# Kernel tuning notes

Measured on AMD Instinct MI355X. Metric: run time of the kernel, lower is better.

The kernel has to match this reference:

```python
import jax, jax.numpy as jnp
import numpy as np

N = 25600          # total nodes
B = 64             # graphs in batch
NPG = N // B       # nodes per graph (400)
K = 16             # in-degree (regular graph)
E = N * K          # edges
D = 128            # hidden dim = out dim
L = 4              # DGN layers
NUM_ATOM = 128


def _linear_init(key, out_s, in_s):
    lim = 1.0 / np.sqrt(in_s)
    return jax.random.uniform(key, (out_s, in_s), jnp.float32, -lim, lim)


def setup_inputs() -> dict:
    key = jax.random.key(0)
    ks = jax.random.split(key, 16)
    node_feat = jax.random.randint(ks[0], (N,), 0, NUM_ATOM)
    # K-regular in-degree graph, edges intra-graph; dst sorted
    dst = jnp.repeat(jnp.arange(N), K)                       # [E]
    src_local = jax.random.randint(ks[1], (E,), 0, NPG)
    src = (dst // NPG) * NPG + src_local                     # same graph as dst
    eig = jax.random.normal(ks[2], (E, 2), jnp.float32)
    snorm_n = jnp.full((N, 1), 1.0 / np.sqrt(NPG), jnp.float32)
    graph_ids = jnp.arange(N) // NPG
    emb = jax.random.normal(ks[3], (NUM_ATOM, D), jnp.float32) * 0.02
    pre_W = jnp.stack([_linear_init(jax.random.fold_in(ks[4], i), D, 2 * D) for i in range(L)])
    pre_b = jnp.zeros((L, D), jnp.float32)
    post_W = jnp.stack([_linear_init(jax.random.fold_in(ks[5], i), D, 5 * D) for i in range(L)])
    post_b = jnp.zeros((L, D), jnp.float32)
    r_W0 = _linear_init(ks[6], 64, 128); r_b0 = jnp.zeros((64,), jnp.float32)
    r_W1 = _linear_init(ks[7], 32, 64);  r_b1 = jnp.zeros((32,), jnp.float32)
    r_W2 = _linear_init(ks[8], 128, 32); r_b2 = jnp.zeros((128,), jnp.float32)
    return dict(node_feat=node_feat, src=src, dst=dst, eig=eig, snorm_n=snorm_n,
                graph_ids=graph_ids, emb=emb, pre_W=pre_W, pre_b=pre_b,
                post_W=post_W, post_b=post_b, r_W0=r_W0, r_b0=r_b0,
                r_W1=r_W1, r_b1=r_b1, r_W2=r_W2, r_b2=r_b2)


def _dgn_layer(h, src, dst, eig, snorm_n, Wp, bp, Wq, bq):
    n = h.shape[0]
    # pretrans on edges: Linear(cat(h_src, h_dst))  [E, D]
    z2 = jnp.concatenate([h[src], h[dst]], axis=-1)
    e = jnp.einsum('ei,oi->eo', z2, Wp) + bp
    seg_sum = lambda v: jax.ops.segment_sum(v, dst, num_segments=n, indices_are_sorted=True)
    s = seg_sum(e)
    mean = s / K
    mx = jax.ops.segment_max(e, dst, num_segments=n, indices_are_sorted=True)
    # directional aggregator (eig_idx=1)
    w = eig[:, 1]
    denom = seg_sum(jnp.abs(w)) + 1e-8                       # [n]
    ew = w / denom[dst]                                      # [E]
    dir_agg = jnp.abs(seg_sum(e * ew[:, None]) - seg_sum(ew)[:, None] * h)
    agg = jnp.concatenate([h, mean, s, mx, dir_agg], axis=-1)  # [n, 5D]
    hn = jnp.einsum('ni,oi->no', agg, Wq) + bq
    hn = hn * snorm_n           # graph_norm
    hn = jax.nn.relu(hn)
    return h + hn               # residual (in_dim == out_dim)


def reference(node_feat, src, dst, eig, snorm_n, graph_ids, emb,
              pre_W, pre_b, post_W, post_b,
              r_W0, r_b0, r_W1, r_b1, r_W2, r_b2):
    h = emb[node_feat]                                       # AtomEncoder
    for i in range(L):
        h = _dgn_layer(h, src, dst, eig, snorm_n, pre_W[i], pre_b[i], post_W[i], post_b[i])
    # mean_nodes per graph (equal-sized graphs)
    hg = jax.ops.segment_sum(h, graph_ids, num_segments=B, indices_are_sorted=True) / NPG
    y = jax.nn.relu(hg @ r_W0.T + r_b0)
    y = jax.nn.relu(y @ r_W1.T + r_b1)
    return y @ r_W2.T + r_b2                                 # [B, 128]
```

## Files before the change

kernel.cpp:

```cpp
#include <hip/hip_runtime.h>
#include <cstddef>

#define NN 25600
#define BB 64
#define NPG 400
#define KK 16
#define LL 4

typedef _Float16 half_t;
typedef _Float16 h8 __attribute__((ext_vector_type(8)));
typedef _Float16 h4 __attribute__((ext_vector_type(4)));
typedef float f32x4 __attribute__((ext_vector_type(4)));

__global__ __launch_bounds__(256) void prep_k(const float* __restrict__ preW,
                                              const float* __restrict__ preb,
                                              const float* __restrict__ postW,
                                              half_t* __restrict__ WpreH,
                                              half_t* __restrict__ WpreL,
                                              float* __restrict__ bpre,
                                              half_t* __restrict__ WpostH,
                                              half_t* __restrict__ WpostL) {
  int idx = blockIdx.x * 256 + threadIdx.x;
  const int n1 = LL * 256 * 128;
  const int n2 = n1 + LL * 256;
  const int n3 = n2 + LL * 128 * 512;
  if (idx < n1) {
    int l = idx / 32768;
    int q = idx % 32768;
    int j = q & 7, lane = (q >> 3) & 63, kc = (q >> 9) & 3, c16 = q >> 11;
    int col = c16 * 16 + (lane & 15);
    int k = kc * 32 + (lane >> 4) * 8 + j;
    float v = (col < 128) ? preW[(size_t)l * 32768 + (size_t)col * 256 + k]
                          : preW[(size_t)l * 32768 + (size_t)(col - 128) * 256 + 128 + k];
    half_t hi = (half_t)v;
    WpreH[idx] = hi;
    WpreL[idx] = (half_t)(v - (float)hi);
  } else if (idx < n2) {
    int r = idx - n1;
    int l = r / 256, o = r % 256;
    bpre[r] = (o < 128) ? 0.f : preb[l * 128 + (o - 128)];
  } else if (idx < n3) {
    int r = idx - n2;
    int l = r / 65536;
    int q = r % 65536;
    int j = q & 7, lane = (q >> 3) & 63, kc = (q >> 9) & 15, c16 = q >> 13;
    int col = c16 * 16 + (lane & 15);
    int k = kc * 32 + (lane >> 4) * 8 + j;
    int jblk = k >> 7, kk = k & 127;
    const float* base = postW + (size_t)l * 128 * 640 + (size_t)col * 640;
    float v;
    if (jblk == 0)      v = base[kk];
    else if (jblk == 1) v = base[128 + kk] * (1.f / 16.f) + base[256 + kk];
    else if (jblk == 2) v = base[384 + kk];
    else                v = base[512 + kk];
    half_t hi = (half_t)v;
    WpostH[r] = hi;
    WpostL[r] = (half_t)(v - (float)hi);
  }
}

__global__ __launch_bounds__(256) void embed_k(const int* __restrict__ nf,
                                               const float* __restrict__ emb,
                                               float* __restrict__ hf,
                                               half_t* __restrict__ Hh,
                                               half_t* __restrict__ Hl) {
  int idx = blockIdx.x * 256 + threadIdx.x;
  int n = idx >> 5;
  int d4 = idx & 31;
  int a = nf[n];
  float4 v = *(const float4*)(emb + (size_t)a * 128 + d4 * 4);
  *(float4*)(hf + (size_t)n * 128 + d4 * 4) = v;
  h4 hi, lo;
  const float* vp = &v.x;
#pragma unroll
  for (int j = 0; j < 4; ++j) {
    half_t h = (half_t)vp[j];
    hi[j] = h;
    lo[j] = (half_t)(vp[j] - (float)h);
  }
  *(h4*)(Hh + (size_t)n * 128 + d4 * 4) = hi;
  *(h4*)(Hl + (size_t)n * 128 + d4 * 4) = lo;
}

__global__ __launch_bounds__(256) void pre_gemm_k(const half_t* __restrict__ Ah_g,
                                                  const half_t* __restrict__ Al_g,
                                                  const half_t* __restrict__ Wh_g,
                                                  const half_t* __restrict__ Wl_g,
                                                  const float* __restrict__ bias,
                                                  float* __restrict__ outF) {
  __shared__ half_t Ahs[64][132];
  __shared__ half_t Als[64][132];
  const int tid = threadIdx.x;
  const int bid = blockIdx.x;
  const int swz = (bid & 7) * 50 + (bid >> 3);
  const int r0 = swz * 64;
  const int by8 = blockIdx.y * 8;
  const int wid = tid >> 6, lane = tid & 63;
  const int wm = wid >> 1, wn = wid & 1;
  const int lr = lane & 15, lk = (lane >> 4) * 8;
  f32x4 acc[2][4] = {};

  {
    const int row = tid >> 2;
#pragma unroll
    for (int s = 0; s < 4; ++s) {
      const int koff = (tid & 3) * 8 + s * 32;
      const size_t g = (size_t)(r0 + row) * 128 + koff;
      *(h8*)&Ahs[row][koff] = *(const h8*)(Ah_g + g);
      *(h8*)&Als[row][koff] = *(const h8*)(Al_g + g);
    }
  }
  __syncthreads();

#pragma unroll
  for (int kc = 0; kc < 4; ++kc) {
    h8 af[2][2];
#pragma unroll
    for (int mi = 0; mi < 2; ++mi) {
      const int r = wm * 32 + mi * 16 + lr;
      af[mi][0] = *(const h8*)&Ahs[r][kc * 32 + lk];
      af[mi][1] = *(const h8*)&Als[r][kc * 32 + lk];
    }
#pragma unroll
    for (int nj = 0; nj < 4; ++nj) {
      const size_t fi = ((size_t)((by8 + wn * 4 + nj) * 4 + kc) * 64 + lane) * 8;
      const h8 b0v = *(const h8*)(Wh_g + fi);
      const h8 b1v = *(const h8*)(Wl_g + fi);
#pragma unroll
      for (int mi = 0; mi < 2; ++mi) {
        acc[mi][nj] = __builtin_amdgcn_mfma_f32_16x16x32_f16(af[mi][0], b0v, acc[mi][nj], 0, 0, 0);
        acc[mi][nj] = __builtin_amdgcn_mfma_f32_16x16x32_f16(af[mi][0], b1v, acc[mi][nj], 0, 0, 0);
        acc[mi][nj] = __builtin_amdgcn_mfma_f32_16x16x32_f16(af[mi][1], b0v, acc[mi][nj], 0, 0, 0);
      }
    }
  }
#pragma unroll
  for (int mi = 0; mi < 2; ++mi) {
    const int rowb = r0 + wm * 32 + mi * 16 + (lane >> 4) * 4;
#pragma unroll
    for (int nj = 0; nj < 4; ++nj) {
      const int col = by8 * 16 + wn * 64 + nj * 16 + lr;
      const float bv = bias[col];
#pragma unroll
      for (int q = 0; q < 4; ++q) {
        outF[(size_t)(rowb + q) * 256 + col] = acc[mi][nj][q] + bv;
      }
    }
  }
}

__global__ __launch_bounds__(256) void agg_post_k(const float* __restrict__ pre,
                                                  const int* __restrict__ src,
                                                  const float* __restrict__ eig,
                                                  const half_t* __restrict__ Hh,
                                                  const half_t* __restrict__ Hl,
                                                  const half_t* __restrict__ Wh,
                                                  const half_t* __restrict__ Wl,
                                                  const float* __restrict__ bias,
                                                  const float* __restrict__ snorm,
                                                  float* __restrict__ Hf,
                                                  half_t* __restrict__ Oh,
                                                  half_t* __restrict__ Ol) {
  __shared__ half_t Ah[32][392];
  __shared__ half_t Al[32][392];
  const int tid = threadIdx.x;
  const int bid = blockIdx.x;
  const int swz = (bid & 7) * 100 + (bid >> 3);
  const int r0 = swz * 32;
  const int wid = tid >> 6, lane = tid & 63;
  const int wm = wid >> 1, wn = wid & 1;
  const int lr = lane & 15, lk = (lane >> 4) * 8;

  for (int i = 0; i < 8; ++i) {
    const int lrow = wid * 8 + i;
    const int n = r0 + lrow;
    const int ebase = n * KK;
    float wv[KK];
    int sv[KK];
    float denom = 0.f;
#pragma unroll
    for (int e = 0; e < KK; ++e) {
      wv[e] = eig[(size_t)(ebase + e) * 2 + 1];
      sv[e] = src[ebase + e];
      denom += fabsf(wv[e]);
    }
    denom += 1e-8f;
    const float inv = 1.f / denom;
    float sum_ew = 0.f;
#pragma unroll
    for (int e = 0; e < KK; ++e) {
      wv[e] *= inv;
      sum_ew += wv[e];
    }
    float sA0 = 0.f, sA1 = 0.f, wA0 = 0.f, wA1 = 0.f;
    float mA0 = -3.402823466e+38f, mA1 = -3.402823466e+38f;
#pragma unroll
    for (int e = 0; e < KK; ++e) {
      const float* ap = pre + (size_t)sv[e] * 256;
      const float a0 = ap[lane];
      const float a1 = ap[64 + lane];
      sA0 += a0;
      sA1 += a1;
      wA0 = fmaf(wv[e], a0, wA0);
      wA1 = fmaf(wv[e], a1, wA1);
      mA0 = fmaxf(mA0, a0);
      mA1 = fmaxf(mA1, a1);
    }
    const float b0 = pre[(size_t)n * 256 + 128 + lane];
    const float b1 = pre[(size_t)n * 256 + 192 + lane];
    const float h0 = Hf[(size_t)n * 128 + lane];
    const float h1 = Hf[(size_t)n * 128 + 64 + lane];
    const int d0 = lane, d1 = lane + 64;
    auto wr = [&](int kcol, float v) {
      const half_t hi = (half_t)v;
      Ah[lrow][kcol] = hi;
      Al[lrow][kcol] = (half_t)(v - (float)hi);
    };
    wr(d0, sA0 + 16.f * b0);
    wr(d1, sA1 + 16.f * b1);
    wr(128 + d0, mA0 + b0);
    wr(128 + d1, mA1 + b1);
    wr(256 + d0, fabsf(wA0 + sum_ew * (b0 - h0)));
    wr(256 + d1, fabsf(wA1 + sum_ew * (b1 - h1)));
  }

  const int frow = r0 + wm * 16 + lr;
  h8 afh[4][2];
#pragma unroll
  for (int hc = 0; hc < 4; ++hc) {
    afh[hc][0] = *(const h8*)(Hh + (size_t)frow * 128 + hc * 32 + lk);
    afh[hc][1] = *(const h8*)(Hl + (size_t)frow * 128 + hc * 32 + lk);
  }

  __syncthreads();

  f32x4 acc[4] = {};
  const int arow = wm * 16 + lr;
#pragma unroll
  for (int kc = 0; kc < 16; ++kc) {
    h8 a0, a1;
    if (kc < 4) {
      a0 = afh[kc & 3][0];
      a1 = afh[kc & 3][1];
    } else {
      a0 = *(const h8*)&Ah[arow][(kc - 4) * 32 + lk];
      a1 = *(const h8*)&Al[arow][(kc - 4) * 32 + lk];
    }
#pragma unroll
    for (int nj = 0; nj < 4; ++nj) {
      const size_t fi = ((size_t)((wn * 4 + nj) * 16 + kc) * 64 + lane) * 8;
      const h8 b0v = *(const h8*)(Wh + fi);
      const h8 b1v = *(const h8*)(Wl + fi);
      acc[nj] = __builtin_amdgcn_mfma_f32_16x16x32_f16(a0, b0v, acc[nj], 0, 0, 0);
      acc[nj] = __builtin_amdgcn_mfma_f32_16x16x32_f16(a0, b1v, acc[nj], 0, 0, 0);
      acc[nj] = __builtin_amdgcn_mfma_f32_16x16x32_f16(a1, b0v, acc[nj], 0, 0, 0);
    }
  }

  const int rowb = r0 + wm * 16 + (lane >> 4) * 4;
#pragma unroll
  for (int nj = 0; nj < 4; ++nj) {
    const int col = wn * 64 + nj * 16 + lr;
    const float bv = bias[col];
#pragma unroll
    for (int q = 0; q < 4; ++q) {
      const int r = rowb + q;
      float a = acc[nj][q] + bv;
      a *= snorm[r];
      a = fmaxf(a, 0.f);
      const float hn = Hf[(size_t)r * 128 + col] + a;
      Hf[(size_t)r * 128 + col] = hn;
      const half_t hi = (half_t)hn;
      Oh[(size_t)r * 128 + col] = hi;
      Ol[(size_t)r * 128 + col] = (half_t)(hn - (float)hi);
    }
  }
}

__global__ __launch_bounds__(256) void reduce_mlp_k(const float* __restrict__ h,
                                                    const float* __restrict__ W0, const float* __restrict__ b0,
                                                    const float* __restrict__ W1, const float* __restrict__ b1,
                                                    const float* __restrict__ W2, const float* __restrict__ b2,
                                                    float* __restrict__ out) {
  __shared__ float hgs[128];
  __shared__ float red[128];
  __shared__ float y0s[64];
  __shared__ float y1s[32];
  __shared__ float wb[64 * 130];
  const int g = blockIdx.x;
  const int t = threadIdx.x;
  {
    const int d = t & 127, hf = t >> 7;
    const float* p = h + ((size_t)g * NPG + (size_t)hf * 200) * 128 + d;
    float acc = 0.f;
    for (int i = 0; i < 200; ++i) acc += p[(size_t)i * 128];
    if (hf) red[d] = acc;
    __syncthreads();
    if (!hf) hgs[d] = (acc + red[d]) * (1.f / (float)NPG);
  }
  __syncthreads();
  for (int idx = t; idx < 64 * 128; idx += 256) {
    wb[(idx >> 7) * 130 + (idx & 127)] = W0[idx];
  }
  __syncthreads();
  if (t < 64) {
    float a = b0[t];
    const float* w = &wb[t * 130];
    for (int k = 0; k < 128; ++k) a = fmaf(hgs[k], w[k], a);
    y0s[t] = fmaxf(a, 0.f);
  }
  __syncthreads();
  for (int idx = t; idx < 32 * 64; idx += 256) {
    wb[(idx >> 6) * 66 + (idx & 63)] = W1[idx];
  }
  __syncthreads();
  if (t < 32) {
    float a = b1[t];
    const float* w = &wb[t * 66];
    for (int k = 0; k < 64; ++k) a = fmaf(y0s[k], w[k], a);
    y1s[t] = fmaxf(a, 0.f);
  }
  __syncthreads();
  for (int idx = t; idx < 128 * 32; idx += 256) {
    wb[(idx >> 5) * 34 + (idx & 31)] = W2[idx];
  }
  __syncthreads();
  if (t < 128) {
    float a = b2[t];
    const float* w = &wb[t * 34];
    for (int k = 0; k < 32; ++k) a = fmaf(y1s[k], w[k], a);
    out[(size_t)g * 128 + t] = a;
  }
}

extern "C" void kernel_launch(void* const* d_in, const int* in_sizes, int n_in,
                              void* d_out, int out_size, void* d_ws, size_t ws_size,
                              hipStream_t stream) {
  const int* node_feat = (const int*)d_in[0];
  const int* src = (const int*)d_in[1];
  const float* eig = (const float*)d_in[3];
  const float* snorm = (const float*)d_in[4];
  const float* emb = (const float*)d_in[6];
  const float* preW = (const float*)d_in[7];
  const float* preb = (const float*)d_in[8];
  const float* postW = (const float*)d_in[9];
  const float* postb = (const float*)d_in[10];
  const float* rW0 = (const float*)d_in[11];
  const float* rb0 = (const float*)d_in[12];
  const float* rW1 = (const float*)d_in[13];
  const float* rb1 = (const float*)d_in[14];
  const float* rW2 = (const float*)d_in[15];
  const float* rb2 = (const float*)d_in[16];
  float* out = (float*)d_out;

  half_t* Hh = (half_t*)d_ws;
  half_t* Hl = Hh + (size_t)NN * 128;
  float* Hf = (float*)(Hl + (size_t)NN * 128);
  float* pre = Hf + (size_t)NN * 128;
  half_t* WpreH = (half_t*)(pre + (size_t)NN * 256);
  half_t* WpreL = WpreH + (size_t)LL * 32768;
  half_t* WpostH = WpreL + (size_t)LL * 32768;
  half_t* WpostL = WpostH + (size_t)LL * 65536;
  float* bpre = (float*)(WpostL + (size_t)LL * 65536);

  prep_k<<<1540, 256, 0, stream>>>(preW, preb, postW, WpreH, WpreL, bpre, WpostH, WpostL);
  embed_k<<<(NN * 32) / 256, 256, 0, stream>>>(node_feat, emb, Hf, Hh, Hl);

  for (int l = 0; l < LL; ++l) {
    pre_gemm_k<<<dim3(NN / 64, 2), 256, 0, stream>>>(
        Hh, Hl, WpreH + (size_t)l * 32768, WpreL + (size_t)l * 32768,
        bpre + (size_t)l * 256, pre);
    agg_post_k<<<NN / 32, 256, 0, stream>>>(
        pre, src, eig, Hh, Hl, WpostH + (size_t)l * 65536, WpostL + (size_t)l * 65536,
        postb + (size_t)l * 128, snorm, Hf, Hh, Hl);
  }

  reduce_mlp_k<<<BB, 256, 0, stream>>>(Hf, rW0, rb0, rW1, rb1, rW2, rb2, out);
}
```

Before: 279.1 us.

## Halve agg_post rows per block and vectorize edge and feature loads

The aggregation and post-GEMM kernel now processes 16 rows per block instead of 32, doubling the grid to 1600 blocks, with each wave owning a 32-column slice of the output. Edge src indices and eigenvector weights are read with int4/float4 loads, and per-lane pre-activation reads become float2 for adjacent columns, writing LDS in h2 pairs. This aims to raise occupancy and parallelism across the gather phase and to cut the number of memory instructions. The cost is that the post weights are re-read by twice as many blocks, and each block has less MFMA work to amortize that.

Measured after the change: 266.0 us. -4.7%, faster.

```diff
diff --git a/kernel.cpp b/kernel.cpp
--- a/kernel.cpp
+++ b/kernel.cpp
@@ -10,6 +10,7 @@
 typedef _Float16 half_t;
 typedef _Float16 h8 __attribute__((ext_vector_type(8)));
 typedef _Float16 h4 __attribute__((ext_vector_type(4)));
+typedef _Float16 h2 __attribute__((ext_vector_type(2)));
 typedef float f32x4 __attribute__((ext_vector_type(4)));
 
 __global__ __launch_bounds__(256) void prep_k(const float* __restrict__ preW,
@@ -161,29 +162,42 @@
                                                   float* __restrict__ Hf,
                                                   half_t* __restrict__ Oh,
                                                   half_t* __restrict__ Ol) {
-  __shared__ half_t Ah[32][392];
-  __shared__ half_t Al[32][392];
+  __shared__ half_t Ah[16][392];
+  __shared__ half_t Al[16][392];
   const int tid = threadIdx.x;
   const int bid = blockIdx.x;
-  const int swz = (bid & 7) * 100 + (bid >> 3);
-  const int r0 = swz * 32;
+  const int swz = (bid & 7) * 200 + (bid >> 3);
+  const int r0 = swz * 16;
   const int wid = tid >> 6, lane = tid & 63;
-  const int wm = wid >> 1, wn = wid & 1;
+  const int wn = wid;
   const int lr = lane & 15, lk = (lane >> 4) * 8;
 
-  for (int i = 0; i < 8; ++i) {
-    const int lrow = wid * 8 + i;
+  for (int i = 0; i < 4; ++i) {
+    const int lrow = wid * 4 + i;
     const int n = r0 + lrow;
-    const int ebase = n * KK;
+    int sv[KK];
     float wv[KK];
-    int sv[KK];
+    {
+      const int4* sp4 = (const int4*)(src + (size_t)n * KK);
+      const float4* ep4 = (const float4*)(eig + (size_t)n * KK * 2);
+#pragma unroll
+      for (int t = 0; t < 4; ++t) {
+        const int4 s4 = sp4[t];
+        sv[4 * t + 0] = s4.x;
+        sv[4 * t + 1] = s4.y;
+        sv[4 * t + 2] = s4.z;
+        sv[4 * t + 3] = s4.w;
+      }
+#pragma unroll
+      for (int t = 0; t < 8; ++t) {
+        const float4 e4 = ep4[t];
+        wv[2 * t + 0] = e4.y;
+        wv[2 * t + 1] = e4.w;
+      }
+    }
     float denom = 0.f;
 #pragma unroll
-    for (int e = 0; e < KK; ++e) {
-      wv[e] = eig[(size_t)(ebase + e) * 2 + 1];
-      sv[e] = src[ebase + e];
-      denom += fabsf(wv[e]);
-    }
+    for (int e = 0; e < KK; ++e) denom += fabsf(wv[e]);
     denom += 1e-8f;
     const float inv = 1.f / denom;
     float sum_ew = 0.f;
@@ -196,35 +210,32 @@
     float mA0 = -3.402823466e+38f, mA1 = -3.402823466e+38f;
 #pragma unroll
     for (int e = 0; e < KK; ++e) {
-      const float* ap = pre + (size_t)sv[e] * 256;
-      const float a0 = ap[lane];
-      const float a1 = ap[64 + lane];
-      sA0 += a0;
-      sA1 += a1;
-      wA0 = fmaf(wv[e], a0, wA0);
-      wA1 = fmaf(wv[e], a1, wA1);
-      mA0 = fmaxf(mA0, a0);
-      mA1 = fmaxf(mA1, a1);
-    }
-    const float b0 = pre[(size_t)n * 256 + 128 + lane];
-    const float b1 = pre[(size_t)n * 256 + 192 + lane];
-    const float h0 = Hf[(size_t)n * 128 + lane];
-    const float h1 = Hf[(size_t)n * 128 + 64 + lane];
-    const int d0 = lane, d1 = lane + 64;
-    auto wr = [&](int kcol, float v) {
-      const half_t hi = (half_t)v;
-      Ah[lrow][kcol] = hi;
-      Al[lrow][kcol] = (half_t)(v - (float)hi);
+      const float2 a = *(const float2*)(pre + (size_t)sv[e] * 256 + 2 * lane);
+      sA0 += a.x;
+      sA1 += a.y;
+      wA0 = fmaf(wv[e], a.x, wA0);
+      wA1 = fmaf(wv[e], a.y, wA1);
+      mA0 = fmaxf(mA0, a.x);
+      mA1 = fmaxf(mA1, a.y);
+    }
+    const float2 b = *(const float2*)(pre + (size_t)n * 256 + 128 + 2 * lane);
+    const float2 hv = *(const float2*)(Hf + (size_t)n * 128 + 2 * lane);
+    const int d0 = 2 * lane;
+    auto wr2 = [&](int kcol, float v0, float v1) {
+      h2 hi, lo;
+      hi[0] = (half_t)v0;
+      hi[1] = (half_t)v1;
+      lo[0] = (half_t)(v0 - (float)hi[0]);
+      lo[1] = (half_t)(v1 - (float)hi[1]);
+      *(h2*)&Ah[lrow][kcol] = hi;
+      *(h2*)&Al[lrow][kcol] = lo;
     };
-    wr(d0, sA0 + 16.f * b0);
-    wr(d1, sA1 + 16.f * b1);
-    wr(128 + d0, mA0 + b0);
-    wr(128 + d1, mA1 + b1);
-    wr(256 + d0, fabsf(wA0 + sum_ew * (b0 - h0)));
-    wr(256 + d1, fabsf(wA1 + sum_ew * (b1 - h1)));
-  }
-
-  const int frow = r0 + wm * 16 + lr;
+    wr2(d0, sA0 + 16.f * b.x, sA1 + 16.f * b.y);
+    wr2(128 + d0, mA0 + b.x, mA1 + b.y);
+    wr2(256 + d0, fabsf(wA0 + sum_ew * (b.x - hv.x)), fabsf(wA1 + sum_ew * (b.y - hv.y)));
+  }
+
+  const int frow = r0 + lr;
   h8 afh[4][2];
 #pragma unroll
   for (int hc = 0; hc < 4; ++hc) {
@@ -234,8 +245,7 @@
 
   __syncthreads();
 
-  f32x4 acc[4] = {};
-  const int arow = wm * 16 + lr;
+  f32x4 acc[2] = {};
 #pragma unroll
   for (int kc = 0; kc < 16; ++kc) {
     h8 a0, a1;
@@ -243,12 +253,12 @@
       a0 = afh[kc & 3][0];
       a1 = afh[kc & 3][1];
     } else {
-      a0 = *(const h8*)&Ah[arow][(kc - 4) * 32 + lk];
-      a1 = *(const h8*)&Al[arow][(kc - 4) * 32 + lk];
-    }
-#pragma unroll
-    for (int nj = 0; nj < 4; ++nj) {
-      const size_t fi = ((size_t)((wn * 4 + nj) * 16 + kc) * 64 + lane) * 8;
+      a0 = *(const h8*)&Ah[lr][(kc - 4) * 32 + lk];
+      a1 = *(const h8*)&Al[lr][(kc - 4) * 32 + lk];
+    }
+#pragma unroll
+    for (int nj = 0; nj < 2; ++nj) {
+      const size_t fi = ((size_t)((wn * 2 + nj) * 16 + kc) * 64 + lane) * 8;
       const h8 b0v = *(const h8*)(Wh + fi);
       const h8 b1v = *(const h8*)(Wl + fi);
       acc[nj] = __builtin_amdgcn_mfma_f32_16x16x32_f16(a0, b0v, acc[nj], 0, 0, 0);
@@ -257,10 +267,10 @@
     }
   }
 
-  const int rowb = r0 + wm * 16 + (lane >> 4) * 4;
-#pragma unroll
-  for (int nj = 0; nj < 4; ++nj) {
-    const int col = wn * 64 + nj * 16 + lr;
+  const int rowb = r0 + (lane >> 4) * 4;
+#pragma unroll
+  for (int nj = 0; nj < 2; ++nj) {
+    const int col = wn * 32 + nj * 16 + lr;
     const float bv = bias[col];
 #pragma unroll
     for (int q = 0; q < 4; ++q) {
@@ -370,7 +380,7 @@
     pre_gemm_k<<<dim3(NN / 64, 2), 256, 0, stream>>>(
         Hh, Hl, WpreH + (size_t)l * 32768, WpreL + (size_t)l * 32768,
         bpre + (size_t)l * 256, pre);
-    agg_post_k<<<NN / 32, 256, 0, stream>>>(
+    agg_post_k<<<NN / 16, 256, 0, stream>>>(
         pre, src, eig, Hh, Hl, WpostH + (size_t)l * 65536, WpostL + (size_t)l * 65536,
         postb + (size_t)l * 128, snorm, Hf, Hh, Hl);
   }
```
